# Kernel optimization log

Measured on AMD Instinct MI355X. Metric: run time of the kernel, lower is better.

## Reference

```python
import jax, jax.numpy as jnp
import numpy as np

TWO_PI = 2.0 * np.pi


def quat2mat3(q):
    # q: (B,4) (w,x,y,z), normalized internally -> (B,3,3)
    q = q / jnp.linalg.norm(q, axis=-1, keepdims=True)
    w, x, y, z = q[:, 0], q[:, 1], q[:, 2], q[:, 3]
    R = jnp.stack([
        1 - 2 * (y * y + z * z), 2 * (x * y - w * z), 2 * (x * z + w * y),
        2 * (x * y + w * z), 1 - 2 * (x * x + z * z), 2 * (y * z - w * x),
        2 * (x * z - w * y), 2 * (y * z + w * x), 1 - 2 * (x * x + y * y),
    ], axis=-1).reshape(-1, 3, 3)
    return R


def se3(R, t):
    # R: (B,3,3), t: (B,3) -> (B,4,4)
    B = R.shape[0]
    top = jnp.concatenate([R, t[:, :, None]], axis=2)            # (B,3,4)
    bottom = jnp.broadcast_to(jnp.array([[0., 0., 0., 1.]], R.dtype), (B, 1, 4))
    return jnp.concatenate([top, bottom], axis=1)


def mat2quat(R):
    # batched rotation matrix -> quaternion (w,x,y,z), branchless 4-case Shepperd
    R00, R01, R02 = R[:, 0, 0], R[:, 0, 1], R[:, 0, 2]
    R10, R11, R12 = R[:, 1, 0], R[:, 1, 1], R[:, 1, 2]
    R20, R21, R22 = R[:, 2, 0], R[:, 2, 1], R[:, 2, 2]
    tr = R00 + R11 + R22
    t0 = 1.0 + tr
    t1 = 1.0 + R00 - R11 - R22
    t2 = 1.0 - R00 + R11 - R22
    t3 = 1.0 - R00 - R11 + R22
    q0 = jnp.stack([t0, R21 - R12, R02 - R20, R10 - R01], axis=-1)
    q1 = jnp.stack([R21 - R12, t1, R01 + R10, R02 + R20], axis=-1)
    q2 = jnp.stack([R02 - R20, R01 + R10, t2, R12 + R21], axis=-1)
    q3 = jnp.stack([R10 - R01, R02 + R20, R12 + R21, t3], axis=-1)
    qs = jnp.stack([q0, q1, q2, q3], axis=1)   # (B,4,4)
    ts = jnp.stack([t0, t1, t2, t3], axis=1)   # (B,4)
    diag = jnp.stack([R00, R11, R22], axis=1)
    sel = jnp.where(tr > 0, 0, 1 + jnp.argmax(diag, axis=1))
    q = jnp.take_along_axis(qs, sel[:, None, None].astype(jnp.int32).repeat(4, 2), axis=1)[:, 0]
    t = jnp.take_along_axis(ts, sel[:, None].astype(jnp.int32), axis=1)[:, 0]
    return q * (0.5 / jnp.sqrt(jnp.clip(t, 1e-12)))[:, None]


def quat_mul(a, b):
    aw, av = a[:, :1], a[:, 1:]
    bw, bv = b[:, :1], b[:, 1:]
    w = aw * bw - jnp.sum(av * bv, axis=1, keepdims=True)
    v = aw * bv + bw * av + jnp.cross(av, bv)
    return jnp.concatenate([w, v], axis=1)


def quat_distance(q, r):
    r_inv = jnp.concatenate([r[:, :1], -r[:, 1:]], axis=1)  # conjugate (unit quats)
    d = quat_mul(q, r_inv)
    return 2.0 * jnp.arctan2(jnp.linalg.norm(d[:, 1:], axis=1), jnp.abs(d[:, 0]))


def smooth_l1(x, y):
    d = jnp.abs(x - y)
    return jnp.where(d < 1.0, 0.5 * d * d, d - 0.5)


def _rand_se3(key, B):
    kq, kt = jax.random.split(key)
    q = jax.random.normal(kq, (B, 4), jnp.float32)
    R = quat2mat3(q)
    t = jax.random.normal(kt, (B, 3), jnp.float32)
    return se3(R, t)


def setup_inputs() -> dict:
    key = jax.random.key(0)
    B, N = 8, 1_000_000
    k1, k2, k3, k4, k5 = jax.random.split(key, 5)
    return {
        "pred_translation": 0.1 * jax.random.normal(k1, (B, 3), jnp.float32),
        "pred_rotation": jax.random.normal(k2, (B, 4), jnp.float32),
        "pcs": 20.0 * jax.random.normal(k3, (B, N, 3), jnp.float32),
        "gt_T_to_camera": _rand_se3(k4, B),
        "init_T_to_camera": _rand_se3(k5, B),
        "mask": jnp.ones((B, N), jnp.int32),
    }


def reference(pred_translation, pred_rotation, pcs, gt_T_to_camera, init_T_to_camera, mask):
    W_T, W_R, W_PC, W_QN = 1.0, 0.5, 0.5, 0.5
    B = pcs.shape[0]

    # quat norm loss on raw predicted quaternion
    norm_sq = jnp.sum(pred_rotation ** 2, axis=1)
    qn_loss = jnp.mean((norm_sq - 1.0) ** 2)

    # T_pred = trans(t) @ rot(q)  -> (B,4,4)
    T_t = se3(jnp.broadcast_to(jnp.eye(3, dtype=pcs.dtype), (B, 3, 3)), pred_translation)
    T_r = se3(quat2mat3(pred_rotation), jnp.zeros((B, 3), pcs.dtype))
    T_pred = jnp.einsum('bij,bjk->bik', T_t, T_r)

    # T_gt_expected = inv(T_pred) @ init_T
    T_gt_exp = jnp.einsum('bij,bjk->bik', jnp.linalg.inv(T_pred), init_T_to_camera)
    p_t = T_gt_exp[:, :3, 3]
    p_R = T_gt_exp[:, :3, :3]
    g_t = gt_T_to_camera[:, :3, 3]
    g_R = gt_T_to_camera[:, :3, :3]

    # translation: smooth-L1, sum over axes, mean over batch
    t_loss = jnp.mean(jnp.sum(smooth_l1(p_t, g_t), axis=1))

    # PC reprojection: RT_total = inv(gt_T) @ [p_R|p_t]
    T_pred2 = se3(p_R, p_t)
    RT = jnp.einsum('bij,bjk->bik', jnp.linalg.inv(gt_T_to_camera), T_pred2)
    pts = jnp.einsum('bij,bnj->bni', RT[:, :3, :3], pcs) + RT[:, None, :3, 3]
    err = jnp.linalg.norm(pts - pcs, axis=2)               # (B,N)
    mf = mask.astype(pcs.dtype)
    pc_loss = jnp.mean(jnp.sum(err * mf, axis=1) / jnp.sum(mf, axis=1))

    # rotation: quaternion geodesic distance between matrix-derived quats
    r_loss = jnp.mean(quat_distance(mat2quat(p_R), mat2quat(g_R)))

    loss = W_T * t_loss + W_R * r_loss + W_PC * pc_loss + W_QN * qn_loss
    return loss
```

## Files before the change

kernel.cpp:

```cpp
#include <hip/hip_runtime.h>
#include <math.h>

struct Pose {
    float M[9], Tt[3], pR[9], pt[3], gR[9], gt[3], qn;
};

__device__ __forceinline__ float smooth_l1f(float x, float y) {
    float d = fabsf(x - y);
    return d < 1.0f ? 0.5f * d * d : d - 0.5f;
}

__device__ void mat2quat_dev(const float* R, float* q) {
    float R00=R[0],R01=R[1],R02=R[2];
    float R10=R[3],R11=R[4],R12=R[5];
    float R20=R[6],R21=R[7],R22=R[8];
    float tr = R00 + R11 + R22;
    float t;
    if (tr > 0.0f) {
        t = 1.0f + tr;
        q[0]=t; q[1]=R21-R12; q[2]=R02-R20; q[3]=R10-R01;
    } else {
        int sel = 1; float best = R00;
        if (R11 > best) { sel = 2; best = R11; }
        if (R22 > best) { sel = 3; }
        if (sel == 1)      { t = 1.0f+R00-R11-R22; q[0]=R21-R12; q[1]=t; q[2]=R01+R10; q[3]=R02+R20; }
        else if (sel == 2) { t = 1.0f-R00+R11-R22; q[0]=R02-R20; q[1]=R01+R10; q[2]=t; q[3]=R12+R21; }
        else               { t = 1.0f-R00-R11+R22; q[0]=R10-R01; q[1]=R02+R20; q[2]=R12+R21; q[3]=t; }
    }
    float s = 0.5f / sqrtf(fmaxf(t, 1e-12f));
    q[0]*=s; q[1]*=s; q[2]*=s; q[3]*=s;
}

__device__ void compute_pose(int b,
                             const float* __restrict__ pred_t,
                             const float* __restrict__ pred_q,
                             const float* __restrict__ gtT,
                             const float* __restrict__ initT,
                             Pose& P)
{
    float tx=pred_t[b*3+0], ty=pred_t[b*3+1], tz=pred_t[b*3+2];
    float q0=pred_q[b*4+0], q1=pred_q[b*4+1], q2=pred_q[b*4+2], q3=pred_q[b*4+3];
    float nsq = q0*q0+q1*q1+q2*q2+q3*q3;
    P.qn = (nsq-1.0f)*(nsq-1.0f);
    float inv = rsqrtf(nsq);
    float w=q0*inv, x=q1*inv, y=q2*inv, z=q3*inv;
    float R[9];
    R[0]=1.0f-2.0f*(y*y+z*z); R[1]=2.0f*(x*y-w*z);      R[2]=2.0f*(x*z+w*y);
    R[3]=2.0f*(x*y+w*z);      R[4]=1.0f-2.0f*(x*x+z*z); R[5]=2.0f*(y*z-w*x);
    R[6]=2.0f*(x*z-w*y);      R[7]=2.0f*(y*z+w*x);      R[8]=1.0f-2.0f*(x*x+y*y);

    float iR[9], it[3];
    for (int i=0;i<3;i++){
        for (int j=0;j<3;j++){
            iR[i*3+j]=initT[b*16+i*4+j];
            P.gR[i*3+j]=gtT[b*16+i*4+j];
        }
        it[i]=initT[b*16+i*4+3];
        P.gt[i]=gtT[b*16+i*4+3];
    }
    for (int i=0;i<3;i++){
        for (int j=0;j<3;j++)
            P.pR[i*3+j] = R[0+i]*iR[0+j] + R[3+i]*iR[3+j] + R[6+i]*iR[6+j];
        P.pt[i] = R[0+i]*(it[0]-tx) + R[3+i]*(it[1]-ty) + R[6+i]*(it[2]-tz);
    }
    for (int i=0;i<3;i++){
        for (int j=0;j<3;j++)
            P.M[i*3+j] = P.gR[0+i]*P.pR[0+j] + P.gR[3+i]*P.pR[3+j] + P.gR[6+i]*P.pR[6+j];
        P.Tt[i] = P.gR[0+i]*(P.pt[0]-P.gt[0]) + P.gR[3+i]*(P.pt[1]-P.gt[1]) + P.gR[6+i]*(P.pt[2]-P.gt[2]);
    }
    P.M[0]-=1.0f; P.M[4]-=1.0f; P.M[8]-=1.0f;
}

__global__ __launch_bounds__(256) void pc_fused(const float* __restrict__ pcs,
                                                const int* __restrict__ mask,
                                                const float* __restrict__ pred_t,
                                                const float* __restrict__ pred_q,
                                                const float* __restrict__ gtT,
                                                const float* __restrict__ initT,
                                                float* __restrict__ errS,
                                                float* __restrict__ maskS,
                                                int N, int bpb)
{
    int b   = blockIdx.x / bpb;
    int blk = blockIdx.x - b*bpb;
    int t   = threadIdx.x;

    __shared__ float sMT[12];
    __shared__ float sP[3072];
    float4* sP4 = (float4*)sP;

    if (t == 0) {
        Pose P;
        compute_pose(b, pred_t, pred_q, gtT, initT, P);
        #pragma unroll
        for (int k=0;k<9;k++) sMT[k]=P.M[k];
        sMT[9]=P.Tt[0]; sMT[10]=P.Tt[1]; sMT[11]=P.Tt[2];
    }
    __syncthreads();
    float m00=sMT[0], m01=sMT[1], m02=sMT[2];
    float m10=sMT[3], m11=sMT[4], m12=sMT[5];
    float m20=sMT[6], m21=sMT[7], m22=sMT[8];
    float t0 =sMT[9], t1 =sMT[10], t2 =sMT[11];

    const float4* pbase = (const float4*)(pcs + (size_t)b * N * 3);
    const int*    mbase = mask + (size_t)b * N;
    float esum = 0.0f, msum = 0.0f;

    int ntiles = N >> 10;
    for (int tile = blk; tile < ntiles; tile += bpb) {
        const float4* src = pbase + (size_t)tile * 768;
        __syncthreads();
        sP4[t      ] = src[t      ];
        sP4[t + 256] = src[t + 256];
        sP4[t + 512] = src[t + 512];
        __syncthreads();
        int gbase = tile << 10;
        #pragma unroll
        for (int k=0;k<4;k++){
            int p = t + (k<<8);
            float x = sP[3*p], y = sP[3*p+1], z = sP[3*p+2];
            float mm = (float)mbase[gbase + p];
            float dx = m00*x + m01*y + m02*z + t0;
            float dy = m10*x + m11*y + m12*z + t1;
            float dz = m20*x + m21*y + m22*z + t2;
            esum += mm * sqrtf(dx*dx + dy*dy + dz*dz);
            msum += mm;
        }
    }
    if (blk == 0) {
        for (int p = (ntiles<<10) + t; p < N; p += 256) {
            float x = pcs[((size_t)b*N + p)*3 + 0];
            float y = pcs[((size_t)b*N + p)*3 + 1];
            float z = pcs[((size_t)b*N + p)*3 + 2];
            float mm = (float)mbase[p];
            float dx = m00*x + m01*y + m02*z + t0;
            float dy = m10*x + m11*y + m12*z + t1;
            float dz = m20*x + m21*y + m22*z + t2;
            esum += mm*sqrtf(dx*dx+dy*dy+dz*dz);
            msum += mm;
        }
    }

    for (int off=32; off>0; off>>=1){
        esum += __shfl_down(esum, off);
        msum += __shfl_down(msum, off);
    }
    __shared__ float sE[4], sM[4];
    int lane = t & 63, wid = t >> 6;
    if (lane==0){ sE[wid]=esum; sM[wid]=msum; }
    __syncthreads();
    if (t==0){
        errS [blockIdx.x] = sE[0]+sE[1]+sE[2]+sE[3];
        maskS[blockIdx.x] = sM[0]+sM[1]+sM[2]+sM[3];
    }
}

__global__ void finish_kernel(const float* __restrict__ errS,
                              const float* __restrict__ maskS,
                              const float* __restrict__ pred_t,
                              const float* __restrict__ pred_q,
                              const float* __restrict__ gtT,
                              const float* __restrict__ initT,
                              float* __restrict__ out, int B, int bpb)
{
    int t = threadIdx.x, lane = t & 63, w = t >> 6;
    __shared__ double sPC[4];
    double acc = 0.0;
    for (int b = w; b < B; b += 4) {
        float e=0.0f, m=0.0f;
        for (int k=lane; k<bpb; k+=64){ e += errS[b*bpb+k]; m += maskS[b*bpb+k]; }
        for (int off=32; off>0; off>>=1){
            e += __shfl_down(e, off);
            m += __shfl_down(m, off);
        }
        if (lane==0) acc += (double)e / (double)m;
    }
    if (lane==0) sPC[w] = acc;

    float partial = 0.0f;
    if (t < B) {
        Pose P;
        compute_pose(t, pred_t, pred_q, gtT, initT, P);
        float t_term = smooth_l1f(P.pt[0],P.gt[0]) + smooth_l1f(P.pt[1],P.gt[1])
                     + smooth_l1f(P.pt[2],P.gt[2]);
        float qp[4], qg[4];
        mat2quat_dev(P.pR,qp); mat2quat_dev(P.gR,qg);
        float dw  = qp[0]*qg[0] + qp[1]*qg[1] + qp[2]*qg[2] + qp[3]*qg[3];
        float cx  = qp[2]*qg[3]-qp[3]*qg[2];
        float cy  = qp[3]*qg[1]-qp[1]*qg[3];
        float cz  = qp[1]*qg[2]-qp[2]*qg[1];
        float dvx = -qp[0]*qg[1] + qg[0]*qp[1] - cx;
        float dvy = -qp[0]*qg[2] + qg[0]*qp[2] - cy;
        float dvz = -qp[0]*qg[3] + qg[0]*qp[3] - cz;
        float r_term = 2.0f*atan2f(sqrtf(dvx*dvx+dvy*dvy+dvz*dvz), fabsf(dw));
        partial = (1.0f*t_term + 0.5f*r_term + 0.5f*P.qn) / (float)B;
    }
    if (w==0)
        for (int off=32; off>0; off>>=1) partial += __shfl_down(partial, off);
    __syncthreads();
    if (t==0){
        double pc = sPC[0]+sPC[1]+sPC[2]+sPC[3];
        out[0] = partial + 0.5f * (float)(pc / (double)B);
    }
}

extern "C" void kernel_launch(void* const* d_in, const int* in_sizes, int n_in,
                              void* d_out, int out_size, void* d_ws, size_t ws_size,
                              hipStream_t stream)
{
    const float* pred_t = (const float*)d_in[0];
    const float* pred_q = (const float*)d_in[1];
    const float* pcs    = (const float*)d_in[2];
    const float* gtT    = (const float*)d_in[3];
    const float* initT  = (const float*)d_in[4];
    const int*   mask   = (const int*)d_in[5];

    int B = in_sizes[0] / 3;
    int N = in_sizes[2] / (B * 3);

    int bpb = 256;
    float* errS  = (float*)d_ws;
    float* maskS = errS + B*bpb;
    float* out   = (float*)d_out;

    pc_fused<<<B*bpb, 256, 0, stream>>>(pcs, mask, pred_t, pred_q, gtT, initT,
                                        errS, maskS, N, bpb);
    finish_kernel<<<1, 256, 0, stream>>>(errS, maskS, pred_t, pred_q, gtT, initT,
                                         out, B, bpb);
}
```

Baseline: 32.39 us.

## Split points into contiguous chunks per block with register-staged double buffering

Each block now owns a contiguous chunk of points instead of striding over 1024-point tiles. Tiles shrink to 512 points, and the next tile's point and mask data are prefetched into registers as float4/int4 while the current tile is computed from a double-buffered shared array. Mask values are now loaded vectorized into shared memory, and the arithmetic uses explicit FMAs. This is meant to overlap global loads with compute and widen mask loads. In exchange it adds more register pressure and partial-tile bounds checks, and it assumes the chunk is aligned to 4 elements so the float4 and int4 casts are valid.

```diff
diff --git a/kernel.cpp b/kernel.cpp
--- a/kernel.cpp
+++ b/kernel.cpp
@@ -71,6 +71,10 @@
     P.M[0]-=1.0f; P.M[4]-=1.0f; P.M[8]-=1.0f;
 }
 
+#define TP  512
+#define F4T 384
+#define M4T 128
+
 __global__ __launch_bounds__(256) void pc_fused(const float* __restrict__ pcs,
                                                 const int* __restrict__ mask,
                                                 const float* __restrict__ pred_t,
@@ -79,15 +83,29 @@
                                                 const float* __restrict__ initT,
                                                 float* __restrict__ errS,
                                                 float* __restrict__ maskS,
-                                                int N, int bpb)
+                                                int N, int bpb, int chunk)
 {
     int b   = blockIdx.x / bpb;
     int blk = blockIdx.x - b*bpb;
     int t   = threadIdx.x;
 
     __shared__ float sMT[12];
-    __shared__ float sP[3072];
-    float4* sP4 = (float4*)sP;
+    __shared__ float sP[2][F4T*4];
+    __shared__ float sK[2][TP];
+    __shared__ float sE[4], sM[4];
+
+    int r0 = blk * chunk;
+    if (r0 >= N) {
+        if (t==0){ errS[blockIdx.x]=0.0f; maskS[blockIdx.x]=0.0f; }
+        return;
+    }
+    int my_pts = N - r0; if (my_pts > chunk) my_pts = chunk;
+    int nt    = (my_pts + TP - 1) / TP;
+    int my_f4 = (my_pts * 3) >> 2;
+    int my_m4 = my_pts >> 2;
+
+    const float4* pf4 = (const float4*)pcs  + ((size_t)b*N + r0)*3/4;
+    const int4*   mi4 = (const int4*)  mask + ((size_t)b*N + r0)/4;
 
     if (t == 0) {
         Pose P;
@@ -96,56 +114,75 @@
         for (int k=0;k<9;k++) sMT[k]=P.M[k];
         sMT[9]=P.Tt[0]; sMT[10]=P.Tt[1]; sMT[11]=P.Tt[2];
     }
+
+    float4 rA = make_float4(0,0,0,0);
+    float4 rB = make_float4(0,0,0,0);
+    float4 rM = make_float4(0,0,0,0);
+
+    auto stage = [&](int ti) {
+        int fbase = ti * F4T;
+        bool full = (ti*TP + TP <= my_pts);
+        if (full) {
+            rA = pf4[fbase + t];
+            if (t < 128) {
+                rB = pf4[fbase + 256 + t];
+                int4 m = mi4[ti*M4T + t];
+                rM = make_float4((float)m.x,(float)m.y,(float)m.z,(float)m.w);
+            }
+        } else {
+            int s0 = fbase + t;
+            rA = (s0 < my_f4) ? pf4[s0] : make_float4(0,0,0,0);
+            if (t < 128) {
+                int s1 = fbase + 256 + t;
+                rB = (s1 < my_f4) ? pf4[s1] : make_float4(0,0,0,0);
+                int s2 = ti*M4T + t;
+                if (s2 < my_m4) {
+                    int4 m = mi4[s2];
+                    rM = make_float4((float)m.x,(float)m.y,(float)m.z,(float)m.w);
+                } else rM = make_float4(0,0,0,0);
+            }
+        }
+    };
+    auto wr = [&](int buf) {
+        ((float4*)sP[buf])[t] = rA;
+        if (t < 128) {
+            ((float4*)sP[buf])[256 + t] = rB;
+            ((float4*)sK[buf])[t]       = rM;
+        }
+    };
+
+    stage(0);
     __syncthreads();
     float m00=sMT[0], m01=sMT[1], m02=sMT[2];
     float m10=sMT[3], m11=sMT[4], m12=sMT[5];
     float m20=sMT[6], m21=sMT[7], m22=sMT[8];
     float t0 =sMT[9], t1 =sMT[10], t2 =sMT[11];
-
-    const float4* pbase = (const float4*)(pcs + (size_t)b * N * 3);
-    const int*    mbase = mask + (size_t)b * N;
+    wr(0);
+    __syncthreads();
+
     float esum = 0.0f, msum = 0.0f;
-
-    int ntiles = N >> 10;
-    for (int tile = blk; tile < ntiles; tile += bpb) {
-        const float4* src = pbase + (size_t)tile * 768;
+    for (int ti = 0; ti < nt; ti++) {
+        int cur = ti & 1;
+        if (ti + 1 < nt) stage(ti + 1);
+        #pragma unroll
+        for (int k = 0; k < 2; k++) {
+            int p = t + (k << 8);
+            float x = sP[cur][3*p], y = sP[cur][3*p+1], z = sP[cur][3*p+2];
+            float mm = sK[cur][p];
+            float dx = fmaf(m00,x, fmaf(m01,y, fmaf(m02,z, t0)));
+            float dy = fmaf(m10,x, fmaf(m11,y, fmaf(m12,z, t1)));
+            float dz = fmaf(m20,x, fmaf(m21,y, fmaf(m22,z, t2)));
+            esum = fmaf(mm, sqrtf(fmaf(dx,dx, fmaf(dy,dy, dz*dz))), esum);
+            msum += mm;
+        }
+        if (ti + 1 < nt) wr(cur ^ 1);
         __syncthreads();
-        sP4[t      ] = src[t      ];
-        sP4[t + 256] = src[t + 256];
-        sP4[t + 512] = src[t + 512];
-        __syncthreads();
-        int gbase = tile << 10;
-        #pragma unroll
-        for (int k=0;k<4;k++){
-            int p = t + (k<<8);
-            float x = sP[3*p], y = sP[3*p+1], z = sP[3*p+2];
-            float mm = (float)mbase[gbase + p];
-            float dx = m00*x + m01*y + m02*z + t0;
-            float dy = m10*x + m11*y + m12*z + t1;
-            float dz = m20*x + m21*y + m22*z + t2;
-            esum += mm * sqrtf(dx*dx + dy*dy + dz*dz);
-            msum += mm;
-        }
-    }
-    if (blk == 0) {
-        for (int p = (ntiles<<10) + t; p < N; p += 256) {
-            float x = pcs[((size_t)b*N + p)*3 + 0];
-            float y = pcs[((size_t)b*N + p)*3 + 1];
-            float z = pcs[((size_t)b*N + p)*3 + 2];
-            float mm = (float)mbase[p];
-            float dx = m00*x + m01*y + m02*z + t0;
-            float dy = m10*x + m11*y + m12*z + t1;
-            float dz = m20*x + m21*y + m22*z + t2;
-            esum += mm*sqrtf(dx*dx+dy*dy+dz*dz);
-            msum += mm;
-        }
     }
 
     for (int off=32; off>0; off>>=1){
         esum += __shfl_down(esum, off);
         msum += __shfl_down(msum, off);
     }
-    __shared__ float sE[4], sM[4];
     int lane = t & 63, wid = t >> 6;
     if (lane==0){ sE[wid]=esum; sM[wid]=msum; }
     __syncthreads();
@@ -218,13 +255,15 @@
     int B = in_sizes[0] / 3;
     int N = in_sizes[2] / (B * 3);
 
-    int bpb = 256;
+    int bpb   = 256;
+    int chunk = (((N + bpb - 1) / bpb) + 3) & ~3;
+
     float* errS  = (float*)d_ws;
     float* maskS = errS + B*bpb;
     float* out   = (float*)d_out;
 
     pc_fused<<<B*bpb, 256, 0, stream>>>(pcs, mask, pred_t, pred_q, gtT, initT,
-                                        errS, maskS, N, bpb);
+                                        errS, maskS, N, bpb, chunk);
     finish_kernel<<<1, 256, 0, stream>>>(errS, maskS, pred_t, pred_q, gtT, initT,
                                          out, B, bpb);
 }
```

After: 31.07 us. -4.1%, faster.
